# Performance work log

Measured on AMD Instinct MI355X. Metric: run time of the kernel, lower is better.

## Reference

```python
import jax, jax.numpy as jnp
import numpy as np

DEPTH, E, F, H, U, I, B = 12, 256, 128, 8, 1000, 1000, 64
HD = E // H  # head dim = 32
N = 2 * F + 1  # seq len = 257


def _ln(x, g, b, eps=1e-5):
    m = jnp.mean(x, axis=-1, keepdims=True)
    v = jnp.var(x, axis=-1, keepdims=True)
    return (x - m) / jnp.sqrt(v + eps) * g + b


def setup_inputs() -> dict:
    key = jax.random.key(0)
    ks = jax.random.split(key, 16)
    s = 0.02  # weight scale for numeric sanity
    inp = {
        "user": jax.random.randint(ks[0], (B, 1), 0, U, dtype=jnp.int64) if jax.config.jax_enable_x64 else jax.random.randint(ks[0], (B, 1), 0, U).astype(jnp.int32),
        "item": jax.random.randint(ks[1], (B, 1), 0, I).astype(jnp.int32),
        "user_table": jax.random.normal(ks[2], (E, U, F), jnp.float32) * s,
        "item_table": jax.random.normal(ks[3], (E, I, F), jnp.float32) * s,
        "cls_token": jax.random.normal(ks[4], (1, 1, E), jnp.float32),
        "positions": jax.random.normal(ks[5], (N, E), jnp.float32) * s,
        "ln1_g": jnp.ones((DEPTH, E), jnp.float32),
        "ln1_b": jnp.zeros((DEPTH, E), jnp.float32),
        "Wq": jax.random.normal(ks[6], (DEPTH, E, E), jnp.float32) * s,
        "bq": jnp.zeros((DEPTH, E), jnp.float32),
        "Wk": jax.random.normal(ks[7], (DEPTH, E, E), jnp.float32) * s,
        "bk": jnp.zeros((DEPTH, E), jnp.float32),
        "Wv": jax.random.normal(ks[8], (DEPTH, E, E), jnp.float32) * s,
        "bv": jnp.zeros((DEPTH, E), jnp.float32),
        "Wo": jax.random.normal(ks[9], (DEPTH, E, E), jnp.float32) * s,
        "bo": jnp.zeros((DEPTH, E), jnp.float32),
        "ln2_g": jnp.ones((DEPTH, E), jnp.float32),
        "ln2_b": jnp.zeros((DEPTH, E), jnp.float32),
        "W1": jax.random.normal(ks[10], (DEPTH, E, 4 * E), jnp.float32) * s,
        "b1": jnp.zeros((DEPTH, 4 * E), jnp.float32),
        "W2": jax.random.normal(ks[11], (DEPTH, 4 * E, E), jnp.float32) * s,
        "b2": jnp.zeros((DEPTH, E), jnp.float32),
        "head_g": jnp.ones((E,), jnp.float32),
        "head_b": jnp.zeros((E,), jnp.float32),
        "head_W": jax.random.normal(ks[12], (E, 1), jnp.float32) * s,
        "head_bias": jnp.zeros((1,), jnp.float32),
    }
    return inp


def _forward(user, item, user_table, item_table, cls_token, positions,
             ln1_g, ln1_b, Wq, bq, Wk, bk, Wv, bv, Wo, bo,
             ln2_g, ln2_b, W1, b1, W2, b2, head_g, head_b, head_W, head_bias):
    uid = user[:, 0]
    iid = item[:, 0]
    b = uid.shape[0]
    # emb_size parallel embedding lookups, cat over table axis, then transpose:
    # x_user[b, f, e] = user_table[e, uid[b], f]  -> (b, F, E)
    xu = jnp.transpose(user_table[:, uid, :], (1, 2, 0))
    xi = jnp.transpose(item_table[:, iid, :], (1, 2, 0))
    cls = jnp.broadcast_to(cls_token, (b, 1, E))
    x = jnp.concatenate([cls, xu, xi], axis=1) + positions  # (b, N, E)

    def block(x, p):
        g1, be1, wq, bq_, wk, bk_, wv, bv_, wo, bo_, g2, be2, w1, bb1, w2, bb2 = p
        h = _ln(x, g1, be1)

        def heads(w, bias):
            y = h @ w + bias  # (b, N, E)
            return y.reshape(b, N, H, HD).transpose(0, 2, 1, 3)  # (b, H, N, HD)

        q, k, v = heads(wq, bq_), heads(wk, bk_), heads(wv, bv_)
        energy = jnp.einsum('bhqd,bhkd->bhqk', q, k)  # NOTE: unscaled pre-softmax
        att = jax.nn.softmax(energy, axis=-1) / jnp.sqrt(jnp.float32(E))  # post-softmax scaling quirk
        o = jnp.einsum('bhqk,bhkd->bhqd', att, v)
        o = o.transpose(0, 2, 1, 3).reshape(b, N, E)
        x = x + (o @ wo + bo_)
        h2 = _ln(x, g2, be2)
        ff = jax.nn.gelu(h2 @ w1 + bb1, approximate=False) @ w2 + bb2
        return x + ff, None

    x, _ = jax.lax.scan(block, x, (ln1_g, ln1_b, Wq, bq, Wk, bk, Wv, bv, Wo, bo,
                                   ln2_g, ln2_b, W1, b1, W2, b2))
    pooled = jnp.mean(x, axis=1)  # (b, E)
    return _ln(pooled, head_g, head_b) @ head_W + head_bias  # (b, 1)


def reference(user, item, user_table, item_table, cls_token, positions,
              ln1_g, ln1_b, Wq, bq, Wk, bk, Wv, bv, Wo, bo,
              ln2_g, ln2_b, W1, b1, W2, b2, head_g, head_b, head_W, head_bias):
    return _forward(user, item, user_table, item_table, cls_token, positions,
                    ln1_g, ln1_b, Wq, bq, Wk, bk, Wv, bv, Wo, bo,
                    ln2_g, ln2_b, W1, b1, W2, b2, head_g, head_b, head_W, head_bias)
```

## Files before the change

### kernel.cpp

```cpp
#include <hip/hip_runtime.h>
#include <hip/hip_fp16.h>
#include <math.h>

constexpr int DEPTH = 12;
constexpr int E     = 256;
constexpr int H     = 8;
constexpr int HD    = 32;
constexpr int N     = 257;
constexpr int B     = 64;
constexpr int BN    = B * N;
constexpr int BNP   = 16512;
constexpr int FFD   = 1024;
constexpr int UCNT  = 1000;
constexpr int Fdim  = 128;

enum { EPI_RESID = 1, EPI_GELU = 2, EPI_QKV = 3, EPI_RESID_LN = 4 };

typedef _Float16 f16x8 __attribute__((ext_vector_type(8)));
typedef _Float16 f16x4 __attribute__((ext_vector_type(4)));
typedef float    f32x4 __attribute__((ext_vector_type(4)));

__device__ __forceinline__ float gelu_exact(float z) {
  return 0.5f * z * (1.0f + erff(z * 0.70710678118654752440f));
}

#define GLOAD_LDS16(g, l) __builtin_amdgcn_global_load_lds( \
    (const __attribute__((address_space(1))) void*)(g),     \
    (__attribute__((address_space(3))) void*)(l), 16, 0, 0)

template<int NV>
__device__ __forceinline__ void wait_vmcnt() {
  static_assert(NV == 0 || NV == 4 || NV == 5, "unsupported vmcnt literal");
  if constexpr (NV == 0)      asm volatile("s_waitcnt vmcnt(0)" ::: "memory");
  else if constexpr (NV == 4) asm volatile("s_waitcnt vmcnt(4)" ::: "memory");
  else                        asm volatile("s_waitcnt vmcnt(5)" ::: "memory");
}

__global__ __launch_bounds__(256) void embed_kernel(
    const int* __restrict__ user, const int* __restrict__ item,
    const float* __restrict__ utab, const float* __restrict__ itab,
    const float* __restrict__ pos, float* __restrict__ x)
{
  __shared__ float tile[32][33];
  const int tx = threadIdx.x, ty = threadIdx.y;
  const int b  = blockIdx.z;
  const int e0 = blockIdx.x * 32;
  const int ft = blockIdx.y;
  const bool isU = (ft < 4);
  const int f0 = (ft & 3) * 32;
  const int id = isU ? user[b] : item[b];
  const float* tab = isU ? utab : itab;
  const int nbase = isU ? 1 : 1 + Fdim;
#pragma unroll
  for (int r = 0; r < 4; ++r) {
    const int e = ty + r * 8;
    tile[e][tx] = tab[((size_t)(e0 + e) * UCNT + id) * Fdim + f0 + tx];
  }
  __syncthreads();
#pragma unroll
  for (int r = 0; r < 4; ++r) {
    const int f = ty + r * 8;
    const int n = nbase + f0 + f;
    x[((size_t)b * N + n) * E + e0 + tx] = tile[tx][f] + pos[(size_t)n * E + e0 + tx];
  }
}

__global__ __launch_bounds__(256) void cls_pad_kernel(
    const float* __restrict__ cls, const float* __restrict__ pos,
    float* __restrict__ x, __half* __restrict__ h)
{
  const int t = blockIdx.x * 256 + threadIdx.x;
  if (blockIdx.y == 0) {
    const int b = t >> 8, e = t & 255;
    x[((size_t)b * N) * E + e] = cls[e] + pos[e];
  } else {
    h[(size_t)BN * E + t] = __float2half(0.0f);
  }
}

__global__ __launch_bounds__(256) void convT_kernel(
    const float* __restrict__ in, __half* __restrict__ out,
    int K, int NC, int NCtot, int ncoff)
{
  __shared__ float tile[32][33];
  const int tx = threadIdx.x, ty = threadIdx.y;
  const int n0 = blockIdx.x * 32, k0 = blockIdx.y * 32;
  const float* ip = in + (size_t)blockIdx.z * K * NC;
  __half* op = out + (size_t)blockIdx.z * NCtot * K;
#pragma unroll
  for (int r = 0; r < 4; ++r) {
    const int kk = ty + r * 8;
    tile[kk][tx] = ip[(size_t)(k0 + kk) * NC + n0 + tx];
  }
  __syncthreads();
#pragma unroll
  for (int r = 0; r < 4; ++r) {
    const int nn = ty + r * 8;
    op[(size_t)(ncoff + n0 + nn) * K + k0 + tx] = __float2half(tile[tx][nn]);
  }
}

__global__ __launch_bounds__(256) void ln_kernel(
    const float* __restrict__ x, __half* __restrict__ y,
    const float* __restrict__ g, const float* __restrict__ b)
{
  const int wave = threadIdx.x >> 6, lane = threadIdx.x & 63;
  const int row  = blockIdx.x * 4 + wave;
  const float4 v = *(const float4*)(x + (size_t)row * E + lane * 4);
  float s = v.x + v.y + v.z + v.w;
  float q = v.x * v.x + v.y * v.y + v.z * v.z + v.w * v.w;
#pragma unroll
  for (int o = 32; o > 0; o >>= 1) { s += __shfl_xor(s, o); q += __shfl_xor(q, o); }
  const float mean = s * (1.0f / 256.0f);
  const float var  = q * (1.0f / 256.0f) - mean * mean;
  const float rstd = rsqrtf(var + 1e-5f);
  const float4 gg = *(const float4*)(g + lane * 4);
  const float4 bb = *(const float4*)(b + lane * 4);
  __half2 h0 = __floats2half2_rn((v.x - mean) * rstd * gg.x + bb.x,
                                 (v.y - mean) * rstd * gg.y + bb.y);
  __half2 h1 = __floats2half2_rn((v.z - mean) * rstd * gg.z + bb.z,
                                 (v.w - mean) * rstd * gg.w + bb.w);
  __half2* yp = (__half2*)(y + (size_t)row * E + lane * 4);
  yp[0] = h0; yp[1] = h1;
}

template<int BMC, int BNT, int K, int NCOUT, int EPI>
__global__ __launch_bounds__(256) void gemm_f16(
    const __half* __restrict__ Act, const __half* __restrict__ Wt,
    const float* __restrict__ b0, const float* __restrict__ b1,
    const float* __restrict__ b2,
    const float* __restrict__ lng, const float* __restrict__ lnb,
    __half* __restrict__ hout, void* __restrict__ outp)
{
  constexpr int WAVES_M = BMC / 64;
  constexpr int WAVES_N = 4 / WAVES_M;
  constexpr int MT = 4;
  constexpr int NT = BNT / (16 * WAVES_N);
  constexpr int ASW = (BMC / 16) / 4;
  constexpr int BSW = (BNT / 16) / 4;
  constexpr int NDMA = ASW + BSW;
  constexpr int AHALF = BMC * 32;
  constexpr int BHALF = BNT * 32;
  constexpr int BUF   = AHALF + BHALF;
  constexpr int NSTEP = K / 32;
  static_assert(NT == 4 && MT == 4, "acc shape fixed");

  __shared__ __align__(16) __half smem[2 * BUF];

  const int t = threadIdx.x;
  const int wave = t >> 6, lane = t & 63;
  const int lm = lane & 15, lq = lane >> 4;
  const int col0 = blockIdx.x * BMC;
  const int tok0 = blockIdx.y * BNT;

  const int srow = lane >> 2, sp = lane & 3;
  const __half* ag[ASW]; int aoff[ASW];
#pragma unroll
  for (int i = 0; i < ASW; ++i) {
    const int seg = wave * ASW + i;
    const int row = seg * 16 + srow;
    const int slot = sp ^ ((row >> 1) & 3);
    ag[i] = Wt + (size_t)(col0 + row) * K + slot * 8;
    aoff[i] = seg * 512;
  }
  const __half* bg[BSW]; int boff[BSW];
#pragma unroll
  for (int i = 0; i < BSW; ++i) {
    const int seg = wave * BSW + i;
    const int row = seg * 16 + srow;
    const int slot = sp ^ ((row >> 1) & 3);
    bg[i] = Act + (size_t)(tok0 + row) * K + slot * 8;
    boff[i] = seg * 512;
  }

  auto STAGE = [&](int step, int buf) {
    const int koff = step * 32;
    __half* base = smem + buf * BUF;
#pragma unroll
    for (int i = 0; i < ASW; ++i) GLOAD_LDS16(ag[i] + koff, base + aoff[i]);
#pragma unroll
    for (int i = 0; i < BSW; ++i) GLOAD_LDS16(bg[i] + koff, base + AHALF + boff[i]);
  };

  const int wm = (wave / WAVES_N) * 64;
  const int wn = (wave % WAVES_N) * (16 * NT);

  f32x4 acc[MT][NT];
#pragma unroll
  for (int i = 0; i < MT; ++i)
#pragma unroll
    for (int j = 0; j < NT; ++j) acc[i][j] = (f32x4){0.f, 0.f, 0.f, 0.f};

  STAGE(0, 0);
  for (int s = 0; s < NSTEP; ++s) {
    const int cur = s & 1;
    if (s + 1 < NSTEP) { STAGE(s + 1, cur ^ 1); wait_vmcnt<NDMA>(); }
    else               { wait_vmcnt<0>(); }
    __builtin_amdgcn_s_barrier();
    asm volatile("" ::: "memory");

    const __half* As = smem + cur * BUF;
    const __half* Bs = As + AHALF;
    f16x8 af[MT], bf[NT];
#pragma unroll
    for (int mt = 0; mt < MT; ++mt) {
      const int row = wm + mt * 16 + lm;
      af[mt] = *(const f16x8*)&As[row * 32 + (lq ^ ((row >> 1) & 3)) * 8];
    }
#pragma unroll
    for (int nt = 0; nt < NT; ++nt) {
      const int row = wn + nt * 16 + lm;
      bf[nt] = *(const f16x8*)&Bs[row * 32 + (lq ^ ((row >> 1) & 3)) * 8];
    }
#pragma unroll
    for (int mt = 0; mt < MT; ++mt)
#pragma unroll
      for (int nt = 0; nt < NT; ++nt)
        acc[mt][nt] = __builtin_amdgcn_mfma_f32_16x16x32_f16(af[mt], bf[nt], acc[mt][nt], 0, 0, 0);

    if (s + 1 < NSTEP || EPI == EPI_RESID_LN) {
      __builtin_amdgcn_s_barrier();
      asm volatile("" ::: "memory");
    }
  }

  float br[MT][4];
#pragma unroll
  for (int mt = 0; mt < MT; ++mt) {
    const int cg = col0 + wm + mt * 16 + lq * 4;
    const float* bp;
    if constexpr (EPI == EPI_QKV) {
      const int tsel = cg >> 8;
      bp = (tsel == 0) ? b0 : (tsel == 1 ? b1 : b2);
      bp += (cg & 255);
    } else {
      bp = b0 + cg;
    }
    const float4 bv = *(const float4*)bp;
    br[mt][0] = bv.x; br[mt][1] = bv.y; br[mt][2] = bv.z; br[mt][3] = bv.w;
  }

  if constexpr (EPI == EPI_RESID_LN) {
    float* sred = (float*)smem;
    float* qred = sred + 256;
#pragma unroll
    for (int nt = 0; nt < NT; ++nt) {
      const int tl = wn + nt * 16 + lm;
      const int token = tok0 + tl;
      float* xrow = (float*)outp + (size_t)token * 256;
      float s = 0.f, q = 0.f;
#pragma unroll
      for (int mt = 0; mt < MT; ++mt) {
        const int cg = wm + mt * 16 + lq * 4;
        const float4 xv = *(const float4*)(xrow + cg);
        float v0 = acc[mt][nt][0] + br[mt][0] + xv.x;
        float v1 = acc[mt][nt][1] + br[mt][1] + xv.y;
        float v2 = acc[mt][nt][2] + br[mt][2] + xv.z;
        float v3 = acc[mt][nt][3] + br[mt][3] + xv.w;
        acc[mt][nt][0] = v0; acc[mt][nt][1] = v1;
        acc[mt][nt][2] = v2; acc[mt][nt][3] = v3;
        s += v0 + v1 + v2 + v3;
        q += v0 * v0 + v1 * v1 + v2 * v2 + v3 * v3;
        float4 nv; nv.x = v0; nv.y = v1; nv.z = v2; nv.w = v3;
        *(float4*)(xrow + cg) = nv;
      }
      s += __shfl_xor(s, 16); s += __shfl_xor(s, 32);
      q += __shfl_xor(q, 16); q += __shfl_xor(q, 32);
      if (lq == 0) { sred[wave * 64 + tl] = s; qred[wave * 64 + tl] = q; }
    }
    __syncthreads();
    float4 g4[MT], e4[MT];
#pragma unroll
    for (int mt = 0; mt < MT; ++mt) {
      const int cg = wm + mt * 16 + lq * 4;
      g4[mt] = *(const float4*)(lng + cg);
      e4[mt] = *(const float4*)(lnb + cg);
    }
#pragma unroll
    for (int nt = 0; nt < NT; ++nt) {
      const int tl = wn + nt * 16 + lm;
      const int token = tok0 + tl;
      const float ts = sred[tl] + sred[64 + tl] + sred[128 + tl] + sred[192 + tl];
      const float tq = qred[tl] + qred[64 + tl] + qred[128 + tl] + qred[192 + tl];
      const float mean = ts * (1.0f / 256.0f);
      const float var  = tq * (1.0f / 256.0f) - mean * mean;
      const float rstd = rsqrtf(var + 1e-5f);
      __half* hrow = hout + (size_t)token * 256;
#pragma unroll
      for (int mt = 0; mt < MT; ++mt) {
        const int cg = wm + mt * 16 + lq * 4;
        f16x4 hv;
        hv[0] = (_Float16)((acc[mt][nt][0] - mean) * rstd * g4[mt].x + e4[mt].x);
        hv[1] = (_Float16)((acc[mt][nt][1] - mean) * rstd * g4[mt].y + e4[mt].y);
        hv[2] = (_Float16)((acc[mt][nt][2] - mean) * rstd * g4[mt].z + e4[mt].z);
        hv[3] = (_Float16)((acc[mt][nt][3] - mean) * rstd * g4[mt].w + e4[mt].w);
        *(f16x4*)(hrow + cg) = hv;
      }
    }
  } else {
#pragma unroll
    for (int nt = 0; nt < NT; ++nt) {
      const int token = tok0 + wn + nt * 16 + lm;
      if constexpr (EPI == EPI_RESID) {
        float* xrow = (float*)outp + (size_t)token * 256;
#pragma unroll
        for (int mt = 0; mt < MT; ++mt) {
          const int cg = col0 + wm + mt * 16 + lq * 4;
          float4 xv = *(float4*)(xrow + cg);
          xv.x += acc[mt][nt][0] + br[mt][0];
          xv.y += acc[mt][nt][1] + br[mt][1];
          xv.z += acc[mt][nt][2] + br[mt][2];
          xv.w += acc[mt][nt][3] + br[mt][3];
          *(float4*)(xrow + cg) = xv;
        }
      } else if constexpr (EPI == EPI_GELU) {
        if (token < BN) {
          __half* orow = (__half*)outp + (size_t)token * NCOUT;
#pragma unroll
          for (int mt = 0; mt < MT; ++mt) {
            const int cg = col0 + wm + mt * 16 + lq * 4;
            f16x4 hv;
#pragma unroll
            for (int r = 0; r < 4; ++r)
              hv[r] = (_Float16)gelu_exact(acc[mt][nt][r] + br[mt][r]);
            *(f16x4*)(orow + cg) = hv;
          }
        }
      } else {
        if (token < BN) {
          const unsigned tu = (unsigned)token;
          const unsigned bb = tu / 257u;
          const unsigned nn = tu - bb * 257u;
#pragma unroll
          for (int mt = 0; mt < MT; ++mt) {
            const int cg = col0 + wm + mt * 16 + lq * 4;
            const int tsel = cg >> 8, rc = cg & 255;
            __half* dst = (__half*)outp + (size_t)tsel * (BN * 256)
                        + (((size_t)bb * H + (rc >> 5)) * N + nn) * HD + (rc & 31);
            f16x4 hv;
#pragma unroll
            for (int r = 0; r < 4; ++r)
              hv[r] = (_Float16)(acc[mt][nt][r] + br[mt][r]);
            *(f16x4*)dst = hv;
          }
        }
      }
    }
  }
}

__global__ __launch_bounds__(256) void attn_mfma(
    const __half* __restrict__ q, const __half* __restrict__ k,
    const __half* __restrict__ v, __half* __restrict__ o)
{
  __shared__ __align__(16) __half Ks[272][40];
  __shared__ __align__(16) __half Vt[32][280];

  const int bh = blockIdx.x;
  const int chunk = blockIdx.y;
  const int bb = bh >> 3, hh = bh & 7;
  const int t = threadIdx.x;
  const int wave = t >> 6, lane = t & 63;
  const int lm = lane & 15, lq = lane >> 4;

  const __half* kg = k + (size_t)bh * N * HD;
  const __half* vg = v + (size_t)bh * N * HD;

  const f16x8 zero8 = {0, 0, 0, 0, 0, 0, 0, 0};
  for (int i = t; i < 272 * 4; i += 256) {
    const int n = i >> 2, c8 = (i & 3) * 8;
    f16x8 kv = zero8, vv = zero8;
    if (n < N) {
      kv = *(const f16x8*)(kg + (size_t)n * HD + c8);
      vv = *(const f16x8*)(vg + (size_t)n * HD + c8);
    }
    *(f16x8*)&Ks[n][c8] = kv;
#pragma unroll
    for (int j = 0; j < 8; ++j) Vt[c8 + j][n] = vv[j];
  }
  __syncthreads();

  const int ntiles = chunk ? 8 : 9;
  const int tbase  = chunk ? 9 : 0;
  for (int ti = wave; ti < ntiles; ti += 4) {
    const int q0 = (tbase + ti) * 16;
    const int qg = q0 + lm;
    const int qrow = (qg < N) ? qg : (N - 1);
    const f16x8 bq = *(const f16x8*)(q + ((size_t)bh * N + qrow) * HD + lq * 8);
    f32x4 Ot0 = {0.f, 0.f, 0.f, 0.f}, Ot1 = {0.f, 0.f, 0.f, 0.f};
    float mm = -3.0e38f, ll = 0.0f;

    for (int kt = 0; kt < 17; ++kt) {
      const int k0 = kt * 16;
      const f16x8 ak = *(const f16x8*)&Ks[k0 + lm][lq * 8];
      f32x4 s = __builtin_amdgcn_mfma_f32_16x16x32_f16(ak, bq, (f32x4){0.f, 0.f, 0.f, 0.f}, 0, 0, 0);
      if (k0 == 256) {
        if (lq != 0) s[0] = -3.0e38f;
        s[1] = -3.0e38f; s[2] = -3.0e38f; s[3] = -3.0e38f;
      }
      float tm = fmaxf(fmaxf(s[0], s[1]), fmaxf(s[2], s[3]));
      tm = fmaxf(tm, __shfl_xor(tm, 16));
      tm = fmaxf(tm, __shfl_xor(tm, 32));
      const float mn    = fmaxf(mm, tm);
      const float alpha = __expf(mm - mn);
      const float p0 = __expf(s[0] - mn);
      const float p1 = __expf(s[1] - mn);
      const float p2 = __expf(s[2] - mn);
      const float p3 = __expf(s[3] - mn);
      float ts = p0 + p1 + p2 + p3;
      ts += __shfl_xor(ts, 16);
      ts += __shfl_xor(ts, 32);
      ll = ll * alpha + ts;
      Ot0 *= alpha;
      Ot1 *= alpha;
      const f16x4 pb = {(_Float16)p0, (_Float16)p1, (_Float16)p2, (_Float16)p3};
      const f16x4 av0 = *(const f16x4*)&Vt[lm][k0 + lq * 4];
      const f16x4 av1 = *(const f16x4*)&Vt[16 + lm][k0 + lq * 4];
      Ot0 = __builtin_amdgcn_mfma_f32_16x16x16f16(av0, pb, Ot0, 0, 0, 0);
      Ot1 = __builtin_amdgcn_mfma_f32_16x16x16f16(av1, pb, Ot1, 0, 0, 0);
      mm = mn;
    }

    const float inv = 1.0f / (16.0f * ll);
    if (qg < N) {
      __half* op = o + ((size_t)bb * N + qg) * E + hh * HD + lq * 4;
      __half2* p0 = (__half2*)op;
      p0[0] = __floats2half2_rn(Ot0[0] * inv, Ot0[1] * inv);
      p0[1] = __floats2half2_rn(Ot0[2] * inv, Ot0[3] * inv);
      __half2* p1 = (__half2*)(op + 16);
      p1[0] = __floats2half2_rn(Ot1[0] * inv, Ot1[1] * inv);
      p1[1] = __floats2half2_rn(Ot1[2] * inv, Ot1[3] * inv);
    }
  }
}

__global__ __launch_bounds__(256) void head_kernel(
    const float* __restrict__ x, const float* __restrict__ g,
    const float* __restrict__ bb, const float* __restrict__ hw,
    const float* __restrict__ hbias, float* __restrict__ out)
{
  const int b = blockIdx.x;
  const int e = threadIdx.x;
  const float* xp = x + (size_t)b * N * E + e;
  float s = 0.0f;
  for (int n = 0; n < N; ++n) s += xp[(size_t)n * E];
  const float p = s / 257.0f;

  float ls = p, lq = p * p;
#pragma unroll
  for (int o = 32; o > 0; o >>= 1) { ls += __shfl_xor(ls, o); lq += __shfl_xor(lq, o); }
  __shared__ float sm[4], sv[4], sd[4];
  const int wv = e >> 6, ln = e & 63;
  if (ln == 0) { sm[wv] = ls; sv[wv] = lq; }
  __syncthreads();
  const float mean = (sm[0] + sm[1] + sm[2] + sm[3]) * (1.0f / 256.0f);
  const float var  = (sv[0] + sv[1] + sv[2] + sv[3]) * (1.0f / 256.0f) - mean * mean;
  const float y = (p - mean) * rsqrtf(var + 1e-5f) * g[e] + bb[e];
  float d = y * hw[e];
#pragma unroll
  for (int o = 32; o > 0; o >>= 1) d += __shfl_xor(d, o);
  if (ln == 0) sd[wv] = d;
  __syncthreads();
  if (e == 0) out[b] = sd[0] + sd[1] + sd[2] + sd[3] + hbias[0];
}

extern "C" void kernel_launch(void* const* d_in, const int* in_sizes, int n_in,
                              void* d_out, int out_size, void* d_ws, size_t ws_size,
                              hipStream_t stream)
{
  const int*   user = (const int*)d_in[0];
  const int*   item = (const int*)d_in[1];
  const float* utab = (const float*)d_in[2];
  const float* itab = (const float*)d_in[3];
  const float* cls  = (const float*)d_in[4];
  const float* pos  = (const float*)d_in[5];
  const float* ln1g = (const float*)d_in[6];
  const float* ln1b = (const float*)d_in[7];
  const float* Wq   = (const float*)d_in[8];
  const float* bq   = (const float*)d_in[9];
  const float* Wk   = (const float*)d_in[10];
  const float* bk   = (const float*)d_in[11];
  const float* Wv   = (const float*)d_in[12];
  const float* bv   = (const float*)d_in[13];
  const float* Wo   = (const float*)d_in[14];
  const float* bo   = (const float*)d_in[15];
  const float* ln2g = (const float*)d_in[16];
  const float* ln2b = (const float*)d_in[17];
  const float* W1   = (const float*)d_in[18];
  const float* b1   = (const float*)d_in[19];
  const float* W2   = (const float*)d_in[20];
  const float* b2   = (const float*)d_in[21];
  const float* hg   = (const float*)d_in[22];
  const float* hb   = (const float*)d_in[23];
  const float* hW   = (const float*)d_in[24];
  const float* hbias= (const float*)d_in[25];
  float* out = (float*)d_out;

  float*  x  = (float*)d_ws;
  __half* h  = (__half*)(x + (size_t)BN * E);
  __half* fq = h + (size_t)BNP * E;
  __half* Wqkvt = fq + (size_t)BN * FFD;
  __half* Wot   = Wqkvt + (size_t)DEPTH * 768 * 256;
  __half* W1t   = Wot   + (size_t)DEPTH * 256 * 256;
  __half* W2t   = W1t   + (size_t)DEPTH * 1024 * 256;
  __half* qb = fq;
  __half* kb = fq + (size_t)BN * 256;
  __half* vb = fq + (size_t)2 * BN * 256;

  convT_kernel<<<dim3(8, 8, DEPTH),  dim3(32, 8), 0, stream>>>(Wq, Wqkvt, 256, 256, 768, 0);
  convT_kernel<<<dim3(8, 8, DEPTH),  dim3(32, 8), 0, stream>>>(Wk, Wqkvt, 256, 256, 768, 256);
  convT_kernel<<<dim3(8, 8, DEPTH),  dim3(32, 8), 0, stream>>>(Wv, Wqkvt, 256, 256, 768, 512);
  convT_kernel<<<dim3(8, 8, DEPTH),  dim3(32, 8), 0, stream>>>(Wo, Wot, 256, 256, 256, 0);
  convT_kernel<<<dim3(32, 8, DEPTH), dim3(32, 8), 0, stream>>>(W1, W1t, 256, 1024, 1024, 0);
  convT_kernel<<<dim3(8, 32, DEPTH), dim3(32, 8), 0, stream>>>(W2, W2t, 1024, 256, 256, 0);

  cls_pad_kernel<<<dim3(64, 2), 256, 0, stream>>>(cls, pos, x, h);
  embed_kernel<<<dim3(8, 8, B), dim3(32, 8), 0, stream>>>(user, item, utab, itab, pos, x);
  ln_kernel<<<BN / 4, 256, 0, stream>>>(x, h, ln1g, ln1b);

  for (int L = 0; L < DEPTH; ++L) {
    const float* g1n = ln1g + (size_t)((L + 1) % DEPTH) * E;
    const float* b1n = ln1b + (size_t)((L + 1) % DEPTH) * E;

    gemm_f16<128, 128, 256, 768, EPI_QKV><<<dim3(6, 129), 256, 0, stream>>>(
        h, Wqkvt + (size_t)L * 768 * 256, bq + L * E, bk + L * E, bv + L * E,
        nullptr, nullptr, nullptr, fq);
    attn_mfma<<<dim3(512, 2), 256, 0, stream>>>(qb, kb, vb, h);
    gemm_f16<256, 64, 256, 256, EPI_RESID_LN><<<dim3(1, 257), 256, 0, stream>>>(
        h, Wot + (size_t)L * 256 * 256, bo + L * E, nullptr, nullptr,
        ln2g + L * E, ln2b + L * E, h, x);
    gemm_f16<128, 128, 256, 1024, EPI_GELU><<<dim3(8, 129), 256, 0, stream>>>(
        h, W1t + (size_t)L * 1024 * 256, b1 + (size_t)L * FFD, nullptr, nullptr,
        nullptr, nullptr, nullptr, fq);
    gemm_f16<256, 64, 1024, 256, EPI_RESID_LN><<<dim3(1, 257), 256, 0, stream>>>(
        fq, W2t + (size_t)L * 256 * 1024, b2 + L * E, nullptr, nullptr,
        g1n, b1n, h, x);
  }

  head_kernel<<<B, 256, 0, stream>>>(x, hg, hb, hW, hbias, out);
}
```

Baseline: 1.777 ms.

## Split residual-LayerNorm GEMM into dedicated 512-thread kernel with eight waves

Replaces the 256-thread residual+LayerNorm GEMM variant with a dedicated kernel that runs 8 waves per block. Each wave now covers 64 output columns by 32 tokens instead of 64 by 64, so it holds half the accumulators. Only the first four waves stage activation tiles. The aim is more waves in flight to hide latency in the Wo and W2 GEMMs. In exchange, each staged weight tile is reused less per wave, and the block uses more threads that may limit how many blocks fit per CU.

```diff
diff --git a/kernel.cpp b/kernel.cpp
--- a/kernel.cpp
+++ b/kernel.cpp
@@ -14,7 +14,7 @@
 constexpr int UCNT  = 1000;
 constexpr int Fdim  = 128;
 
-enum { EPI_RESID = 1, EPI_GELU = 2, EPI_QKV = 3, EPI_RESID_LN = 4 };
+enum { EPI_GELU = 2, EPI_QKV = 3 };
 
 typedef _Float16 f16x8 __attribute__((ext_vector_type(8)));
 typedef _Float16 f16x4 __attribute__((ext_vector_type(4)));
@@ -30,10 +30,7 @@
 
 template<int NV>
 __device__ __forceinline__ void wait_vmcnt() {
-  static_assert(NV == 0 || NV == 4 || NV == 5, "unsupported vmcnt literal");
-  if constexpr (NV == 0)      asm volatile("s_waitcnt vmcnt(0)" ::: "memory");
-  else if constexpr (NV == 4) asm volatile("s_waitcnt vmcnt(4)" ::: "memory");
-  else                        asm volatile("s_waitcnt vmcnt(5)" ::: "memory");
+  asm volatile("s_waitcnt vmcnt(%0)" :: "i"(NV) : "memory");
 }
 
 __global__ __launch_bounds__(256) void embed_kernel(
@@ -128,14 +125,10 @@
 __global__ __launch_bounds__(256) void gemm_f16(
     const __half* __restrict__ Act, const __half* __restrict__ Wt,
     const float* __restrict__ b0, const float* __restrict__ b1,
-    const float* __restrict__ b2,
-    const float* __restrict__ lng, const float* __restrict__ lnb,
-    __half* __restrict__ hout, void* __restrict__ outp)
-{
-  constexpr int WAVES_M = BMC / 64;
-  constexpr int WAVES_N = 4 / WAVES_M;
+    const float* __restrict__ b2, void* __restrict__ outp)
+{
   constexpr int MT = 4;
-  constexpr int NT = BNT / (16 * WAVES_N);
+  constexpr int NT = BNT / 32;
   constexpr int ASW = (BMC / 16) / 4;
   constexpr int BSW = (BNT / 16) / 4;
   constexpr int NDMA = ASW + BSW;
@@ -143,7 +136,6 @@
   constexpr int BHALF = BNT * 32;
   constexpr int BUF   = AHALF + BHALF;
   constexpr int NSTEP = K / 32;
-  static_assert(NT == 4 && MT == 4, "acc shape fixed");
 
   __shared__ __align__(16) __half smem[2 * BUF];
 
@@ -182,8 +174,8 @@
     for (int i = 0; i < BSW; ++i) GLOAD_LDS16(bg[i] + koff, base + AHALF + boff[i]);
   };
 
-  const int wm = (wave / WAVES_N) * 64;
-  const int wn = (wave % WAVES_N) * (16 * NT);
+  const int wm = (wave >> 1) * 64;
+  const int wn = (wave & 1) * 64;
 
   f32x4 acc[MT][NT];
 #pragma unroll
@@ -218,7 +210,7 @@
       for (int nt = 0; nt < NT; ++nt)
         acc[mt][nt] = __builtin_amdgcn_mfma_f32_16x16x32_f16(af[mt], bf[nt], acc[mt][nt], 0, 0, 0);
 
-    if (s + 1 < NSTEP || EPI == EPI_RESID_LN) {
+    if (s + 1 < NSTEP) {
       __builtin_amdgcn_s_barrier();
       asm volatile("" ::: "memory");
     }
@@ -240,111 +232,194 @@
     br[mt][0] = bv.x; br[mt][1] = bv.y; br[mt][2] = bv.z; br[mt][3] = bv.w;
   }
 
-  if constexpr (EPI == EPI_RESID_LN) {
-    float* sred = (float*)smem;
-    float* qred = sred + 256;
+#pragma unroll
+  for (int nt = 0; nt < NT; ++nt) {
+    const int token = tok0 + wn + nt * 16 + lm;
+    if constexpr (EPI == EPI_GELU) {
+      if (token < BN) {
+        __half* orow = (__half*)outp + (size_t)token * NCOUT;
+#pragma unroll
+        for (int mt = 0; mt < MT; ++mt) {
+          const int cg = col0 + wm + mt * 16 + lq * 4;
+          f16x4 hv;
+#pragma unroll
+          for (int r = 0; r < 4; ++r)
+            hv[r] = (_Float16)gelu_exact(acc[mt][nt][r] + br[mt][r]);
+          *(f16x4*)(orow + cg) = hv;
+        }
+      }
+    } else {
+      if (token < BN) {
+        const unsigned tu = (unsigned)token;
+        const unsigned bb = tu / 257u;
+        const unsigned nn = tu - bb * 257u;
+#pragma unroll
+        for (int mt = 0; mt < MT; ++mt) {
+          const int cg = col0 + wm + mt * 16 + lq * 4;
+          const int tsel = cg >> 8, rc = cg & 255;
+          __half* dst = (__half*)outp + (size_t)tsel * (BN * 256)
+                      + (((size_t)bb * H + (rc >> 5)) * N + nn) * HD + (rc & 31);
+          f16x4 hv;
+#pragma unroll
+          for (int r = 0; r < 4; ++r)
+            hv[r] = (_Float16)(acc[mt][nt][r] + br[mt][r]);
+          *(f16x4*)dst = hv;
+        }
+      }
+    }
+  }
+}
+
+template<int K>
+__global__ __launch_bounds__(512) void gemm_ln_f16(
+    const __half* __restrict__ Act, const __half* __restrict__ Wt,
+    const float* __restrict__ bias,
+    const float* __restrict__ lng, const float* __restrict__ lnb,
+    __half* __restrict__ hout, float* __restrict__ x)
+{
+  constexpr int MT = 4, NT = 2;
+  constexpr int AHALF = 256 * 32;
+  constexpr int BHALF = 64 * 32;
+  constexpr int BUF   = AHALF + BHALF;
+  constexpr int NSTEP = K / 32;
+
+  __shared__ __align__(16) __half smem[2 * BUF];
+
+  const int t = threadIdx.x;
+  const int w = t >> 6, lane = t & 63;
+  const int lm = lane & 15, lq = lane >> 4;
+  const int tok0 = blockIdx.x * 64;
+
+  const int srow = lane >> 2, sp = lane & 3;
+  const __half* ag[2]; int aoff[2];
+#pragma unroll
+  for (int i = 0; i < 2; ++i) {
+    const int seg = w * 2 + i;
+    const int row = seg * 16 + srow;
+    const int slot = sp ^ ((row >> 1) & 3);
+    ag[i] = Wt + (size_t)row * K + slot * 8;
+    aoff[i] = seg * 512;
+  }
+  const bool sB = (w < 4);
+  const int brow = w * 16 + srow;
+  const int bslot = sp ^ ((brow >> 1) & 3);
+  const __half* bg = Act + (size_t)(tok0 + brow) * K + bslot * 8;
+  const int boff = w * 512;
+
+  auto STAGE = [&](int step, int buf) {
+    const int koff = step * 32;
+    __half* base = smem + buf * BUF;
+#pragma unroll
+    for (int i = 0; i < 2; ++i) GLOAD_LDS16(ag[i] + koff, base + aoff[i]);
+    if (sB) GLOAD_LDS16(bg + koff, base + AHALF + boff);
+  };
+
+  const int wm = (w >> 1) * 64;
+  const int wn = (w & 1) * 32;
+
+  f32x4 acc[MT][NT];
+#pragma unroll
+  for (int i = 0; i < MT; ++i)
+#pragma unroll
+    for (int j = 0; j < NT; ++j) acc[i][j] = (f32x4){0.f, 0.f, 0.f, 0.f};
+
+  STAGE(0, 0);
+  for (int s = 0; s < NSTEP; ++s) {
+    const int cur = s & 1;
+    if (s + 1 < NSTEP) {
+      STAGE(s + 1, cur ^ 1);
+      if (sB) wait_vmcnt<3>(); else wait_vmcnt<2>();
+    } else {
+      wait_vmcnt<0>();
+    }
+    __builtin_amdgcn_s_barrier();
+    asm volatile("" ::: "memory");
+
+    const __half* As = smem + cur * BUF;
+    const __half* Bs = As + AHALF;
+    f16x8 af[MT], bf[NT];
+#pragma unroll
+    for (int mt = 0; mt < MT; ++mt) {
+      const int row = wm + mt * 16 + lm;
+      af[mt] = *(const f16x8*)&As[row * 32 + (lq ^ ((row >> 1) & 3)) * 8];
+    }
 #pragma unroll
     for (int nt = 0; nt < NT; ++nt) {
-      const int tl = wn + nt * 16 + lm;
-      const int token = tok0 + tl;
-      float* xrow = (float*)outp + (size_t)token * 256;
-      float s = 0.f, q = 0.f;
-#pragma unroll
-      for (int mt = 0; mt < MT; ++mt) {
-        const int cg = wm + mt * 16 + lq * 4;
-        const float4 xv = *(const float4*)(xrow + cg);
-        float v0 = acc[mt][nt][0] + br[mt][0] + xv.x;
-        float v1 = acc[mt][nt][1] + br[mt][1] + xv.y;
-        float v2 = acc[mt][nt][2] + br[mt][2] + xv.z;
-        float v3 = acc[mt][nt][3] + br[mt][3] + xv.w;
-        acc[mt][nt][0] = v0; acc[mt][nt][1] = v1;
-        acc[mt][nt][2] = v2; acc[mt][nt][3] = v3;
-        s += v0 + v1 + v2 + v3;
-        q += v0 * v0 + v1 * v1 + v2 * v2 + v3 * v3;
-        float4 nv; nv.x = v0; nv.y = v1; nv.z = v2; nv.w = v3;
-        *(float4*)(xrow + cg) = nv;
-      }
-      s += __shfl_xor(s, 16); s += __shfl_xor(s, 32);
-      q += __shfl_xor(q, 16); q += __shfl_xor(q, 32);
-      if (lq == 0) { sred[wave * 64 + tl] = s; qred[wave * 64 + tl] = q; }
-    }
-    __syncthreads();
-    float4 g4[MT], e4[MT];
+      const int row = wn + nt * 16 + lm;
+      bf[nt] = *(const f16x8*)&Bs[row * 32 + (lq ^ ((row >> 1) & 3)) * 8];
+    }
+#pragma unroll
+    for (int mt = 0; mt < MT; ++mt)
+#pragma unroll
+      for (int nt = 0; nt < NT; ++nt)
+        acc[mt][nt] = __builtin_amdgcn_mfma_f32_16x16x32_f16(af[mt], bf[nt], acc[mt][nt], 0, 0, 0);
+
+    __builtin_amdgcn_s_barrier();
+    asm volatile("" ::: "memory");
+  }
+
+  float br[MT][4];
+#pragma unroll
+  for (int mt = 0; mt < MT; ++mt) {
+    const float4 bv = *(const float4*)(bias + wm + mt * 16 + lq * 4);
+    br[mt][0] = bv.x; br[mt][1] = bv.y; br[mt][2] = bv.z; br[mt][3] = bv.w;
+  }
+
+  float* sred = (float*)smem;
+  float* qred = sred + 256;
+#pragma unroll
+  for (int nt = 0; nt < NT; ++nt) {
+    const int tl = wn + nt * 16 + lm;
+    const int token = tok0 + tl;
+    float* xrow = x + (size_t)token * 256;
+    float s = 0.f, q = 0.f;
 #pragma unroll
     for (int mt = 0; mt < MT; ++mt) {
       const int cg = wm + mt * 16 + lq * 4;
-      g4[mt] = *(const float4*)(lng + cg);
-      e4[mt] = *(const float4*)(lnb + cg);
-    }
-#pragma unroll
-    for (int nt = 0; nt < NT; ++nt) {
-      const int tl = wn + nt * 16 + lm;
-      const int token = tok0 + tl;
-      const float ts = sred[tl] + sred[64 + tl] + sred[128 + tl] + sred[192 + tl];
-      const float tq = qred[tl] + qred[64 + tl] + qred[128 + tl] + qred[192 + tl];
-      const float mean = ts * (1.0f / 256.0f);
-      const float var  = tq * (1.0f / 256.0f) - mean * mean;
-      const float rstd = rsqrtf(var + 1e-5f);
-      __half* hrow = hout + (size_t)token * 256;
-#pragma unroll
-      for (int mt = 0; mt < MT; ++mt) {
-        const int cg = wm + mt * 16 + lq * 4;
-        f16x4 hv;
-        hv[0] = (_Float16)((acc[mt][nt][0] - mean) * rstd * g4[mt].x + e4[mt].x);
-        hv[1] = (_Float16)((acc[mt][nt][1] - mean) * rstd * g4[mt].y + e4[mt].y);
-        hv[2] = (_Float16)((acc[mt][nt][2] - mean) * rstd * g4[mt].z + e4[mt].z);
-        hv[3] = (_Float16)((acc[mt][nt][3] - mean) * rstd * g4[mt].w + e4[mt].w);
-        *(f16x4*)(hrow + cg) = hv;
-      }
-    }
-  } else {
-#pragma unroll
-    for (int nt = 0; nt < NT; ++nt) {
-      const int token = tok0 + wn + nt * 16 + lm;
-      if constexpr (EPI == EPI_RESID) {
-        float* xrow = (float*)outp + (size_t)token * 256;
-#pragma unroll
-        for (int mt = 0; mt < MT; ++mt) {
-          const int cg = col0 + wm + mt * 16 + lq * 4;
-          float4 xv = *(float4*)(xrow + cg);
-          xv.x += acc[mt][nt][0] + br[mt][0];
-          xv.y += acc[mt][nt][1] + br[mt][1];
-          xv.z += acc[mt][nt][2] + br[mt][2];
-          xv.w += acc[mt][nt][3] + br[mt][3];
-          *(float4*)(xrow + cg) = xv;
-        }
-      } else if constexpr (EPI == EPI_GELU) {
-        if (token < BN) {
-          __half* orow = (__half*)outp + (size_t)token * NCOUT;
-#pragma unroll
-          for (int mt = 0; mt < MT; ++mt) {
-            const int cg = col0 + wm + mt * 16 + lq * 4;
-            f16x4 hv;
-#pragma unroll
-            for (int r = 0; r < 4; ++r)
-              hv[r] = (_Float16)gelu_exact(acc[mt][nt][r] + br[mt][r]);
-            *(f16x4*)(orow + cg) = hv;
-          }
-        }
-      } else {
-        if (token < BN) {
-          const unsigned tu = (unsigned)token;
-          const unsigned bb = tu / 257u;
-          const unsigned nn = tu - bb * 257u;
-#pragma unroll
-          for (int mt = 0; mt < MT; ++mt) {
-            const int cg = col0 + wm + mt * 16 + lq * 4;
-            const int tsel = cg >> 8, rc = cg & 255;
-            __half* dst = (__half*)outp + (size_t)tsel * (BN * 256)
-                        + (((size_t)bb * H + (rc >> 5)) * N + nn) * HD + (rc & 31);
-            f16x4 hv;
-#pragma unroll
-            for (int r = 0; r < 4; ++r)
-              hv[r] = (_Float16)(acc[mt][nt][r] + br[mt][r]);
-            *(f16x4*)dst = hv;
-          }
-        }
-      }
+      const float4 xv = *(const float4*)(xrow + cg);
+      float v0 = acc[mt][nt][0] + br[mt][0] + xv.x;
+      float v1 = acc[mt][nt][1] + br[mt][1] + xv.y;
+      float v2 = acc[mt][nt][2] + br[mt][2] + xv.z;
+      float v3 = acc[mt][nt][3] + br[mt][3] + xv.w;
+      acc[mt][nt][0] = v0; acc[mt][nt][1] = v1;
+      acc[mt][nt][2] = v2; acc[mt][nt][3] = v3;
+      s += v0 + v1 + v2 + v3;
+      q += v0 * v0 + v1 * v1 + v2 * v2 + v3 * v3;
+      float4 nv; nv.x = v0; nv.y = v1; nv.z = v2; nv.w = v3;
+      *(float4*)(xrow + cg) = nv;
+    }
+    s += __shfl_xor(s, 16); s += __shfl_xor(s, 32);
+    q += __shfl_xor(q, 16); q += __shfl_xor(q, 32);
+    if (lq == 0) { sred[(w >> 1) * 64 + tl] = s; qred[(w >> 1) * 64 + tl] = q; }
+  }
+  __syncthreads();
+
+  float4 g4[MT], e4[MT];
+#pragma unroll
+  for (int mt = 0; mt < MT; ++mt) {
+    const int cg = wm + mt * 16 + lq * 4;
+    g4[mt] = *(const float4*)(lng + cg);
+    e4[mt] = *(const float4*)(lnb + cg);
+  }
+#pragma unroll
+  for (int nt = 0; nt < NT; ++nt) {
+    const int tl = wn + nt * 16 + lm;
+    const int token = tok0 + tl;
+    const float ts = sred[tl] + sred[64 + tl] + sred[128 + tl] + sred[192 + tl];
+    const float tq = qred[tl] + qred[64 + tl] + qred[128 + tl] + qred[192 + tl];
+    const float mean = ts * (1.0f / 256.0f);
+    const float var  = tq * (1.0f / 256.0f) - mean * mean;
+    const float rstd = rsqrtf(var + 1e-5f);
+    __half* hrow = hout + (size_t)token * 256;
+#pragma unroll
+    for (int mt = 0; mt < MT; ++mt) {
+      const int cg = wm + mt * 16 + lq * 4;
+      f16x4 hv;
+      hv[0] = (_Float16)((acc[mt][nt][0] - mean) * rstd * g4[mt].x + e4[mt].x);
+      hv[1] = (_Float16)((acc[mt][nt][1] - mean) * rstd * g4[mt].y + e4[mt].y);
+      hv[2] = (_Float16)((acc[mt][nt][2] - mean) * rstd * g4[mt].z + e4[mt].z);
+      hv[3] = (_Float16)((acc[mt][nt][3] - mean) * rstd * g4[mt].w + e4[mt].w);
+      *(f16x4*)(hrow + cg) = hv;
     }
   }
 }
@@ -523,17 +598,15 @@
     const float* b1n = ln1b + (size_t)((L + 1) % DEPTH) * E;
 
     gemm_f16<128, 128, 256, 768, EPI_QKV><<<dim3(6, 129), 256, 0, stream>>>(
-        h, Wqkvt + (size_t)L * 768 * 256, bq + L * E, bk + L * E, bv + L * E,
-        nullptr, nullptr, nullptr, fq);
+        h, Wqkvt + (size_t)L * 768 * 256, bq + L * E, bk + L * E, bv + L * E, fq);
     attn_mfma<<<dim3(512, 2), 256, 0, stream>>>(qb, kb, vb, h);
-    gemm_f16<256, 64, 256, 256, EPI_RESID_LN><<<dim3(1, 257), 256, 0, stream>>>(
-        h, Wot + (size_t)L * 256 * 256, bo + L * E, nullptr, nullptr,
+    gemm_ln_f16<256><<<dim3(257), 512, 0, stream>>>(
+        h, Wot + (size_t)L * 256 * 256, bo + L * E,
         ln2g + L * E, ln2b + L * E, h, x);
     gemm_f16<128, 128, 256, 1024, EPI_GELU><<<dim3(8, 129), 256, 0, stream>>>(
-        h, W1t + (size_t)L * 1024 * 256, b1 + (size_t)L * FFD, nullptr, nullptr,
-        nullptr, nullptr, nullptr, fq);
-    gemm_f16<256, 64, 1024, 256, EPI_RESID_LN><<<dim3(1, 257), 256, 0, stream>>>(
-        fq, W2t + (size_t)L * 256 * 1024, b2 + L * E, nullptr, nullptr,
+        h, W1t + (size_t)L * 1024 * 256, b1 + (size_t)L * FFD, nullptr, nullptr, fq);
+    gemm_ln_f16<1024><<<dim3(257), 512, 0, stream>>>(
+        fq, W2t + (size_t)L * 256 * 1024, b2 + L * E,
         g1n, b1n, h, x);
   }
 
```

New measurement: 1.784 ms. About the same (+0.4%).
